# Optimization experiments

Measured on AMD Instinct MI355X. Metric: run time of the kernel, lower is better.

## Reference

```python
import jax, jax.numpy as jnp
import numpy as np


def _sdpa(q, k, v):
    # scaled dot-product attention, no dropout (eval mode)
    d = q.shape[-1]
    s = jnp.einsum('bhqd,bhkd->bhqk', q, k) / jnp.sqrt(jnp.asarray(d, q.dtype))
    a = jax.nn.softmax(s, axis=-1)
    return jnp.einsum('bhqk,bhkd->bhqd', a, v)


def setup_inputs() -> dict:
    key = jax.random.key(0)
    ks = jax.random.split(key, 9)
    BC, H, N, d = 128, 4, 1024, 64
    B, C = 4, 32
    C_ch, l, r, TC = 32, 16, 8, 144
    half_dim = H * d  # 256
    q_t = jax.random.normal(ks[0], (BC, H, N, d), jnp.float32)
    k_t = jax.random.normal(ks[1], (BC, H, N, d), jnp.float32)
    v_t = jax.random.normal(ks[2], (BC, H, N, d), jnp.float32)
    L_n = jax.random.normal(ks[3], (B * N, C_ch, C_ch), jnp.float32)
    slots = jax.random.normal(ks[4], (1, l, half_dim), jnp.float32) * 0.02
    pack_q_w = jax.random.normal(ks[5], (half_dim, half_dim), jnp.float32) * 0.02
    mu_proto_factors = jax.random.normal(ks[6], (l, TC, r), jnp.float32) * 0.02
    spd_beta = jnp.array([0.5], jnp.float32)
    channel_idx = jax.random.randint(ks[7], (C_ch,), 0, TC)
    return dict(q_t=q_t, k_t=k_t, v_t=v_t, L_n=L_n, slots=slots,
                pack_q_w=pack_q_w, mu_proto_factors=mu_proto_factors,
                spd_beta=spd_beta, channel_idx=channel_idx, C=C)


def _spd_distances(L_per_sample, mu_proto_factors, channel_idx):
    # L_per_sample: (B, N, C_ch, C_ch) -> distances (B, l, N)
    B, N, C_ch, _ = L_per_sample.shape
    l = mu_proto_factors.shape[0]
    U_sub = mu_proto_factors[:, channel_idx]            # (l, C_ch, r)
    L_flat = L_per_sample.reshape(B, N, C_ch * C_ch)    # (B, N, C_ch^2)
    L_sqnorm = jnp.sum(L_flat * L_flat, axis=-1)        # (B, N)
    UtU = jnp.einsum('lcr,lcs->lrs', U_sub, U_sub)      # (l, r, r)
    mu_sqnorm = jnp.sum(UtU * UtU, axis=(-2, -1))       # (l,)
    mu_sub = jnp.einsum('lcr,ldr->lcd', U_sub, U_sub)   # (l, C_ch, C_ch)
    mu_flat = mu_sub.reshape(l, C_ch * C_ch)
    cross = jnp.einsum('bni,li->bnl', L_flat, mu_flat)  # (B, N, l)
    dist_sq = L_sqnorm[..., None] + mu_sqnorm[None, None, :] - 2.0 * cross
    dist_sq = jnp.clip(dist_sq, 0.0, None)
    return jnp.sqrt(dist_sq).transpose(0, 2, 1)         # (B, l, N)


def reference(q_t, k_t, v_t, L_n, slots, pack_q_w, mu_proto_factors,
              spd_beta, channel_idx, C):
    BC, H, N, d = q_t.shape
    l = slots.shape[1]
    scale = d ** (-0.5)
    # pack queries: Linear(bias=False) then split heads; slots are shared across batch
    pq = slots[0] @ pack_q_w.T                          # (l, H*d)
    pq = pq.reshape(l, H, d).transpose(1, 0, 2)         # (H, l, d)
    pack_score = jnp.einsum('hld,bhnd->bhln', pq, k_t) * scale  # (BC, H, l, N)
    # SPD geometric bias (L_n is detached in the original)
    B = BC // C
    C_ch = L_n.shape[1]
    L_per_sample = jax.lax.stop_gradient(L_n).reshape(B, N, C_ch, C_ch)
    spd_dist_b = _spd_distances(L_per_sample, mu_proto_factors, channel_idx)  # (B, l, N)
    spd_dist = jnp.repeat(spd_dist_b, C, axis=0)        # (BC, l, N)
    pack_score = pack_score - spd_beta[0] * spd_dist[:, None, :, :]
    pack_attn = jax.nn.softmax(pack_score, axis=-1)
    packed = jnp.einsum('bhln,bhnd->bhld', pack_attn, v_t)  # (BC, H, l, d)
    processed = _sdpa(packed, packed, packed)               # (BC, H, l, d)
    out = _sdpa(q_t, processed, processed)                  # (BC, H, N, d)
    return out
```

## Files before the change

### kernel.cpp

```cpp
#include <hip/hip_runtime.h>
#include <hip/hip_bf16.h>

typedef unsigned short ushort_t;

__device__ __forceinline__ float bf2f(ushort_t u) {
    return __uint_as_float(((unsigned int)u) << 16);
}
__device__ __forceinline__ ushort_t f2bf(float f) {
    __hip_bfloat16 h = __float2bfloat16(f);
    return *reinterpret_cast<ushort_t*>(&h);
}

__global__ __launch_bounds__(256) void k_pq(const float* __restrict__ slots,
                                            const float* __restrict__ W,
                                            float* __restrict__ pq) {
    int l = blockIdx.x, j = threadIdx.x;
    __shared__ float SL[256];
    SL[j] = slots[l * 256 + j];
    __syncthreads();
    const float4* wr = (const float4*)(W + j * 256);
    float acc = 0.f;
#pragma unroll 8
    for (int g = 0; g < 64; ++g) {
        float4 wv = wr[g];
        const float* sl = &SL[g * 4];
        acc += wv.x * sl[0] + wv.y * sl[1] + wv.z * sl[2] + wv.w * sl[3];
    }
    int h = j >> 6, d = j & 63;
    pq[(h * 16 + l) * 64 + d] = acc;
}

__global__ void k_mu(const float* __restrict__ mu,
                     const int* __restrict__ cidx,
                     float* __restrict__ mu_flat,
                     float* __restrict__ mu_sq) {
    int l = blockIdx.x;
    __shared__ float U[256];
    __shared__ float utu[64];
    int t = threadIdx.x;
    {
        int c = t >> 3, r = t & 7;
        U[t] = mu[(l * 144 + cidx[c]) * 8 + r];
    }
    __syncthreads();
#pragma unroll
    for (int i = 0; i < 4; ++i) {
        int e = t + i * 256;
        int c = e >> 5, dd = e & 31;
        float acc = 0.f;
#pragma unroll
        for (int r = 0; r < 8; ++r) acc += U[c * 8 + r] * U[dd * 8 + r];
        mu_flat[l * 1024 + e] = acc;
    }
    if (t < 64) {
        int r = t >> 3, s = t & 7;
        float acc = 0.f;
        for (int c = 0; c < 32; ++c) acc += U[c * 8 + r] * U[c * 8 + s];
        utu[t] = acc;
    }
    __syncthreads();
    if (t == 0) {
        float acc = 0.f;
        for (int i = 0; i < 64; ++i) acc += utu[i] * utu[i];
        mu_sq[l] = acc;
    }
}

__global__ __launch_bounds__(256) void k_dist(const float* __restrict__ Ln,
                                              const float* __restrict__ mu_flat,
                                              const float* __restrict__ mu_sq,
                                              float* __restrict__ dist) {
    int blk = blockIdx.x;
    int nchunk = blk & 63, bs = blk >> 6;
    int t = threadIdx.x;
    int ln = t & 15, rid = t >> 4;
    int n = nchunk * 16 + rid;
    const float4* lr = (const float4*)(Ln + ((size_t)(bs * 1024 + n)) * 1024);
    const float4* mf = (const float4*)mu_flat;
    float lsq = 0.f;
    float cr[16];
#pragma unroll
    for (int l = 0; l < 16; ++l) cr[l] = 0.f;
#pragma unroll 2
    for (int g = 0; g < 16; ++g) {
        float4 lv = lr[g * 16 + ln];
        lsq += lv.x * lv.x + lv.y * lv.y + lv.z * lv.z + lv.w * lv.w;
#pragma unroll
        for (int l = 0; l < 16; ++l) {
            float4 mv = mf[l * 256 + g * 16 + ln];
            cr[l] += lv.x * mv.x + lv.y * mv.y + lv.z * mv.z + lv.w * mv.w;
        }
    }
#pragma unroll
    for (int off = 8; off >= 1; off >>= 1) {
        lsq += __shfl_xor(lsq, off);
#pragma unroll
        for (int l = 0; l < 16; ++l) cr[l] += __shfl_xor(cr[l], off);
    }
    float mycr = cr[0];
#pragma unroll
    for (int l = 1; l < 16; ++l) if (ln == l) mycr = cr[l];
    float d2 = lsq + mu_sq[ln] - 2.f * mycr;
    dist[((size_t)(bs * 16 + ln)) * 1024 + n] = sqrtf(fmaxf(d2, 0.f));
}

__global__ __launch_bounds__(1024) void k_pack2(const float* __restrict__ kt,
                                                const float* __restrict__ vt,
                                                const float* __restrict__ pq,
                                                const float* __restrict__ dist,
                                                const float* __restrict__ beta_p,
                                                float* __restrict__ packed) {
    int bc = blockIdx.x >> 2, h = blockIdx.x & 3;
    int bs = bc >> 5;
    __shared__ __align__(16) float PQ[1024];
    __shared__ __align__(16) ushort_t PB[16 * 1032];
    __shared__ __align__(16) float VST[4096];
    __shared__ float wred[16 * 16];
    __shared__ float gred[16];
    int t = threadIdx.x;
    int lane = t & 63, w = t >> 6;
    PQ[t] = pq[h * 1024 + t];
    float beta = beta_p[0];
    __syncthreads();

    const size_t base = ((size_t)blockIdx.x) * 65536;
    const float4* kr = (const float4*)(kt + base + (size_t)t * 64);
    float sc[16];
#pragma unroll
    for (int l = 0; l < 16; ++l) sc[l] = 0.f;
    for (int g = 0; g < 16; ++g) {
        float4 kv = kr[g];
#pragma unroll
        for (int l = 0; l < 16; ++l) {
            const float* pql = &PQ[l * 64 + g * 4];
            sc[l] += kv.x * pql[0] + kv.y * pql[1] + kv.z * pql[2] + kv.w * pql[3];
        }
    }
#pragma unroll
    for (int l = 0; l < 16; ++l)
        sc[l] = 0.125f * sc[l] - beta * dist[((size_t)(bs * 16 + l)) * 1024 + t];

#pragma unroll
    for (int l = 0; l < 16; ++l) {
        float m = sc[l];
#pragma unroll
        for (int off = 32; off >= 1; off >>= 1) m = fmaxf(m, __shfl_xor(m, off));
        if (lane == 0) wred[l * 16 + w] = m;
    }
    __syncthreads();
    if (t < 16) {
        float m = -1e30f;
#pragma unroll
        for (int w2 = 0; w2 < 16; ++w2) m = fmaxf(m, wred[t * 16 + w2]);
        gred[t] = m;
    }
    __syncthreads();

    float ex[16];
#pragma unroll
    for (int l = 0; l < 16; ++l) {
        ex[l] = __expf(sc[l] - gred[l]);
        float s = ex[l];
#pragma unroll
        for (int off = 32; off >= 1; off >>= 1) s += __shfl_xor(s, off);
        if (lane == 0) wred[l * 16 + w] = s;
    }
    __syncthreads();
    if (t < 16) {
        float s = 0.f;
#pragma unroll
        for (int w2 = 0; w2 < 16; ++w2) s += wred[t * 16 + w2];
        gred[t] = 1.f / s;
    }
    __syncthreads();
#pragma unroll
    for (int l = 0; l < 16; ++l) PB[l * 1032 + t] = f2bf(ex[l] * gred[l]);

    const float4* vr = (const float4*)(vt + base);
    int jg = w >> 2;
    int sl = (w & 3) * 4 + (lane >> 4);
    int dg = lane & 15;
    float4 acc; acc.x = acc.y = acc.z = acc.w = 0.f;
    float4* VST4 = (float4*)VST;
    float4 pre = vr[t];
    for (int ch = 0; ch < 16; ++ch) {
        __syncthreads();
        VST4[t] = pre;
        __syncthreads();
        if (ch < 15) pre = vr[(ch + 1) * 1024 + t];
        const ushort_t* pbp = &PB[sl * 1032 + ch * 64 + jg * 16];
        uint4 pw0 = *(const uint4*)(pbp);
        uint4 pw1 = *(const uint4*)(pbp + 8);
        const float4* vb = VST4 + jg * 256 + dg;
        unsigned wbuf[8] = {pw0.x, pw0.y, pw0.z, pw0.w, pw1.x, pw1.y, pw1.z, pw1.w};
#pragma unroll
        for (int pr = 0; pr < 8; ++pr) {
            float p0 = __uint_as_float(wbuf[pr] << 16);
            float p1 = __uint_as_float(wbuf[pr] & 0xffff0000u);
            float4 v0 = vb[(2 * pr) * 16];
            float4 v1 = vb[(2 * pr + 1) * 16];
            acc.x += p0 * v0.x + p1 * v1.x;
            acc.y += p0 * v0.y + p1 * v1.y;
            acc.z += p0 * v0.z + p1 * v1.z;
            acc.w += p0 * v0.w + p1 * v1.w;
        }
    }
    __syncthreads();
    VST4[jg * 256 + sl * 16 + dg] = acc;
    __syncthreads();
    int l = t >> 6, d = t & 63;
    float sum = VST[l * 64 + d] + VST[1024 + l * 64 + d]
              + VST[2048 + l * 64 + d] + VST[3072 + l * 64 + d];
    packed[((size_t)blockIdx.x) * 1024 + t] = sum;
}

__global__ void k_proc(const float* __restrict__ packed, float* __restrict__ proc) {
    int bh = blockIdx.x;
    __shared__ float P[1024];
    __shared__ float A[256];
    int t = threadIdx.x;
#pragma unroll
    for (int i = 0; i < 4; ++i) P[t + i * 256] = packed[(size_t)bh * 1024 + t + i * 256];
    __syncthreads();
    {
        int i = t >> 4, j = t & 15;
        float acc = 0.f;
#pragma unroll
        for (int dd = 0; dd < 64; ++dd) acc += P[i * 64 + dd] * P[j * 64 + dd];
        A[t] = acc * 0.125f;
    }
    __syncthreads();
    if (t < 16) {
        float m = -1e30f;
#pragma unroll
        for (int j = 0; j < 16; ++j) m = fmaxf(m, A[t * 16 + j]);
        float s = 0.f;
#pragma unroll
        for (int j = 0; j < 16; ++j) { float e = __expf(A[t * 16 + j] - m); A[t * 16 + j] = e; s += e; }
        float inv = 1.f / s;
#pragma unroll
        for (int j = 0; j < 16; ++j) A[t * 16 + j] *= inv;
    }
    __syncthreads();
#pragma unroll
    for (int i = 0; i < 4; ++i) {
        int e = t + i * 256;
        int r = e >> 6, d = e & 63;
        float acc = 0.f;
#pragma unroll
        for (int j = 0; j < 16; ++j) acc += A[r * 16 + j] * P[j * 64 + d];
        proc[(size_t)bh * 1024 + e] = acc;
    }
}

__global__ __launch_bounds__(256) void k_final(const float* __restrict__ qt,
                                               const float* __restrict__ proc,
                                               float* __restrict__ out) {
    int bh = blockIdx.x >> 3, chunk = blockIdx.x & 7;
    __shared__ __align__(16) float P[1024];
    int t = threadIdx.x;
    ((float4*)P)[t] = ((const float4*)(proc + (size_t)bh * 1024))[t];
    __syncthreads();
    int q = t & 3, rid = t >> 2;
    int n0 = chunk * 128 + rid, n1 = n0 + 64;
    const float4* q0 = (const float4*)(qt + ((size_t)bh * 1024 + n0) * 64) + q * 4;
    const float4* q1 = (const float4*)(qt + ((size_t)bh * 1024 + n1) * 64) + q * 4;
    float4 qa0 = q0[0], qa1 = q0[1], qa2 = q0[2], qa3 = q0[3];
    float4 qb0 = q1[0], qb1 = q1[1], qb2 = q1[2], qb3 = q1[3];
    const float4* P4 = (const float4*)P + q * 4;

    float s0[16], s1[16];
#pragma unroll
    for (int j = 0; j < 16; ++j) {
        float4 p0 = P4[j * 16 + 0], p1 = P4[j * 16 + 1];
        float4 p2 = P4[j * 16 + 2], p3 = P4[j * 16 + 3];
        float a = qa0.x * p0.x + qa0.y * p0.y + qa0.z * p0.z + qa0.w * p0.w
                + qa1.x * p1.x + qa1.y * p1.y + qa1.z * p1.z + qa1.w * p1.w
                + qa2.x * p2.x + qa2.y * p2.y + qa2.z * p2.z + qa2.w * p2.w
                + qa3.x * p3.x + qa3.y * p3.y + qa3.z * p3.z + qa3.w * p3.w;
        float b = qb0.x * p0.x + qb0.y * p0.y + qb0.z * p0.z + qb0.w * p0.w
                + qb1.x * p1.x + qb1.y * p1.y + qb1.z * p1.z + qb1.w * p1.w
                + qb2.x * p2.x + qb2.y * p2.y + qb2.z * p2.z + qb2.w * p2.w
                + qb3.x * p3.x + qb3.y * p3.y + qb3.z * p3.z + qb3.w * p3.w;
        a += __shfl_xor(a, 1); a += __shfl_xor(a, 2);
        b += __shfl_xor(b, 1); b += __shfl_xor(b, 2);
        s0[j] = a * 0.125f; s1[j] = b * 0.125f;
    }
    float m0 = s0[0], m1 = s1[0];
#pragma unroll
    for (int j = 1; j < 16; ++j) { m0 = fmaxf(m0, s0[j]); m1 = fmaxf(m1, s1[j]); }
    float t0 = 0.f, t1 = 0.f;
#pragma unroll
    for (int j = 0; j < 16; ++j) {
        s0[j] = __expf(s0[j] - m0); t0 += s0[j];
        s1[j] = __expf(s1[j] - m1); t1 += s1[j];
    }
    float i0 = 1.f / t0, i1 = 1.f / t1;
#pragma unroll
    for (int j = 0; j < 16; ++j) { s0[j] *= i0; s1[j] *= i1; }

    float4 o00, o01, o02, o03, o10, o11, o12, o13;
    o00.x=o00.y=o00.z=o00.w=0.f; o01=o00; o02=o00; o03=o00;
    o10=o00; o11=o00; o12=o00; o13=o00;
#pragma unroll
    for (int j = 0; j < 16; ++j) {
        float4 p0 = P4[j * 16 + 0], p1 = P4[j * 16 + 1];
        float4 p2 = P4[j * 16 + 2], p3 = P4[j * 16 + 3];
        float a = s0[j], b = s1[j];
        o00.x += a * p0.x; o00.y += a * p0.y; o00.z += a * p0.z; o00.w += a * p0.w;
        o01.x += a * p1.x; o01.y += a * p1.y; o01.z += a * p1.z; o01.w += a * p1.w;
        o02.x += a * p2.x; o02.y += a * p2.y; o02.z += a * p2.z; o02.w += a * p2.w;
        o03.x += a * p3.x; o03.y += a * p3.y; o03.z += a * p3.z; o03.w += a * p3.w;
        o10.x += b * p0.x; o10.y += b * p0.y; o10.z += b * p0.z; o10.w += b * p0.w;
        o11.x += b * p1.x; o11.y += b * p1.y; o11.z += b * p1.z; o11.w += b * p1.w;
        o12.x += b * p2.x; o12.y += b * p2.y; o12.z += b * p2.z; o12.w += b * p2.w;
        o13.x += b * p3.x; o13.y += b * p3.y; o13.z += b * p3.z; o13.w += b * p3.w;
    }
    float4* w0 = (float4*)(out + ((size_t)bh * 1024 + n0) * 64) + q * 4;
    float4* w1 = (float4*)(out + ((size_t)bh * 1024 + n1) * 64) + q * 4;
    w0[0] = o00; w0[1] = o01; w0[2] = o02; w0[3] = o03;
    w1[0] = o10; w1[1] = o11; w1[2] = o12; w1[3] = o13;
}

extern "C" void kernel_launch(void* const* d_in, const int* in_sizes, int n_in,
                              void* d_out, int out_size, void* d_ws, size_t ws_size,
                              hipStream_t stream) {
    const float* q     = (const float*)d_in[0];
    const float* k     = (const float*)d_in[1];
    const float* v     = (const float*)d_in[2];
    const float* Ln    = (const float*)d_in[3];
    const float* slots = (const float*)d_in[4];
    const float* W     = (const float*)d_in[5];
    const float* mu    = (const float*)d_in[6];
    const float* beta  = (const float*)d_in[7];
    const int* cidx    = (const int*)d_in[8];

    float* ws     = (float*)d_ws;
    float* pq     = ws;
    float* muf    = ws + 4096;
    float* musq   = ws + 20480;
    float* dist   = ws + 20496;
    float* packed = ws + 86032;
    float* proc   = ws + 610320;

    k_pq   <<<16,   256, 0, stream>>>(slots, W, pq);
    k_mu   <<<16,   256, 0, stream>>>(mu, cidx, muf, musq);
    k_dist <<<256,  256, 0, stream>>>(Ln, muf, musq, dist);
    k_pack2<<<512, 1024, 0, stream>>>(k, v, pq, dist, beta, packed);
    k_proc <<<512,  256, 0, stream>>>(packed, proc);
    k_final<<<4096, 256, 0, stream>>>(q, proc, (float*)d_out);
}
```

Measured before the change: 600.3 us.

## Split pack attention into score and PV kernels, drop max-subtraction softmax

The fused pack kernel is split in two. One kernel computes pack scores over 256-token chunks (2048 blocks), writes the unnormalized exponentials to a global buffer and records partial sums. A second kernel does the P·V product straight from global memory and divides by the summed partials. The k_dist kernel is also re-parallelized with one wavefront per row and lanes split over prototypes. This is meant to raise parallelism and remove the block-wide max/sum reductions and LDS staging, at the cost of an extra global round trip of the probabilities. Skipping the max subtraction risks overflow for large scores, and the probability buffer may fall back to aliasing the output buffer when workspace is small.

```diff
diff --git a/kernel.cpp b/kernel.cpp
--- a/kernel.cpp
+++ b/kernel.cpp
@@ -2,14 +2,6 @@
 #include <hip/hip_bf16.h>
 
 typedef unsigned short ushort_t;
-
-__device__ __forceinline__ float bf2f(ushort_t u) {
-    return __uint_as_float(((unsigned int)u) << 16);
-}
-__device__ __forceinline__ ushort_t f2bf(float f) {
-    __hip_bfloat16 h = __float2bfloat16(f);
-    return *reinterpret_cast<ushort_t*>(&h);
-}
 
 __global__ __launch_bounds__(256) void k_pq(const float* __restrict__ slots,
                                             const float* __restrict__ W,
@@ -71,147 +63,128 @@
                                               const float* __restrict__ mu_sq,
                                               float* __restrict__ dist) {
     int blk = blockIdx.x;
-    int nchunk = blk & 63, bs = blk >> 6;
-    int t = threadIdx.x;
-    int ln = t & 15, rid = t >> 4;
-    int n = nchunk * 16 + rid;
-    const float4* lr = (const float4*)(Ln + ((size_t)(bs * 1024 + n)) * 1024);
-    const float4* mf = (const float4*)mu_flat;
-    float lsq = 0.f;
-    float cr[16];
-#pragma unroll
-    for (int l = 0; l < 16; ++l) cr[l] = 0.f;
-#pragma unroll 2
-    for (int g = 0; g < 16; ++g) {
-        float4 lv = lr[g * 16 + ln];
+    int chunk = blk & 255, bs = blk >> 8;
+    int t = threadIdx.x;
+    int rid = t >> 6, lane = t & 63;
+    int l = lane >> 2, cs = lane & 3;
+    int n = chunk * 4 + rid;
+    const float4* L4 = (const float4*)(Ln + ((size_t)(bs * 1024 + n)) * 1024) + cs * 64;
+    const float4* M4 = (const float4*)mu_flat + l * 256 + cs * 64;
+    float cr = 0.f, lsq = 0.f;
+#pragma unroll 8
+    for (int i = 0; i < 64; ++i) {
+        float4 lv = L4[i];
+        float4 mv = M4[i];
+        cr  += lv.x * mv.x + lv.y * mv.y + lv.z * mv.z + lv.w * mv.w;
         lsq += lv.x * lv.x + lv.y * lv.y + lv.z * lv.z + lv.w * lv.w;
+    }
+    cr  += __shfl_xor(cr, 1);  cr  += __shfl_xor(cr, 2);
+    lsq += __shfl_xor(lsq, 1); lsq += __shfl_xor(lsq, 2);
+    if (cs == 0) {
+        float d2 = lsq + mu_sq[l] - 2.f * cr;
+        dist[((size_t)(bs * 16 + l)) * 1024 + n] = sqrtf(fmaxf(d2, 0.f));
+    }
+}
+
+__global__ __launch_bounds__(256) void k_score(const float* __restrict__ kt,
+                                               const float* __restrict__ pq,
+                                               const float* __restrict__ dist,
+                                               const float* __restrict__ beta_p,
+                                               float* __restrict__ pbuf,
+                                               float* __restrict__ psum) {
+    int bx = blockIdx.x;
+    int nq = bx & 3, bh = bx >> 2;
+    int h = bh & 3;
+    int bs = bh >> 7;
+    __shared__ __align__(16) float PQ[1024];
+    __shared__ float wsum[64];
+    int t = threadIdx.x;
+    int lane = t & 63, w = t >> 6;
+    ((float4*)PQ)[t] = ((const float4*)(pq + h * 1024))[t & 255];
+    float beta = beta_p[0];
+    __syncthreads();
+
+    int n = nq * 256 + t;
+    const float4* kr = (const float4*)(kt + ((size_t)bh) * 65536 + (size_t)n * 64);
+    float sc[16];
+#pragma unroll
+    for (int l = 0; l < 16; ++l) sc[l] = 0.f;
+#pragma unroll
+    for (int gb = 0; gb < 4; ++gb) {
+        float4 kv0 = kr[gb * 4 + 0];
+        float4 kv1 = kr[gb * 4 + 1];
+        float4 kv2 = kr[gb * 4 + 2];
+        float4 kv3 = kr[gb * 4 + 3];
 #pragma unroll
         for (int l = 0; l < 16; ++l) {
-            float4 mv = mf[l * 256 + g * 16 + ln];
-            cr[l] += lv.x * mv.x + lv.y * mv.y + lv.z * mv.z + lv.w * mv.w;
+            const float* p = &PQ[l * 64 + gb * 16];
+            sc[l] += kv0.x * p[0]  + kv0.y * p[1]  + kv0.z * p[2]  + kv0.w * p[3]
+                   + kv1.x * p[4]  + kv1.y * p[5]  + kv1.z * p[6]  + kv1.w * p[7]
+                   + kv2.x * p[8]  + kv2.y * p[9]  + kv2.z * p[10] + kv2.w * p[11]
+                   + kv3.x * p[12] + kv3.y * p[13] + kv3.z * p[14] + kv3.w * p[15];
         }
     }
 #pragma unroll
-    for (int off = 8; off >= 1; off >>= 1) {
-        lsq += __shfl_xor(lsq, off);
-#pragma unroll
-        for (int l = 0; l < 16; ++l) cr[l] += __shfl_xor(cr[l], off);
-    }
-    float mycr = cr[0];
-#pragma unroll
-    for (int l = 1; l < 16; ++l) if (ln == l) mycr = cr[l];
-    float d2 = lsq + mu_sq[ln] - 2.f * mycr;
-    dist[((size_t)(bs * 16 + ln)) * 1024 + n] = sqrtf(fmaxf(d2, 0.f));
-}
-
-__global__ __launch_bounds__(1024) void k_pack2(const float* __restrict__ kt,
-                                                const float* __restrict__ vt,
-                                                const float* __restrict__ pq,
-                                                const float* __restrict__ dist,
-                                                const float* __restrict__ beta_p,
-                                                float* __restrict__ packed) {
-    int bc = blockIdx.x >> 2, h = blockIdx.x & 3;
-    int bs = bc >> 5;
-    __shared__ __align__(16) float PQ[1024];
-    __shared__ __align__(16) ushort_t PB[16 * 1032];
-    __shared__ __align__(16) float VST[4096];
-    __shared__ float wred[16 * 16];
-    __shared__ float gred[16];
+    for (int l = 0; l < 16; ++l) {
+        float e = __expf(0.125f * sc[l] - beta * dist[((size_t)(bs * 16 + l)) * 1024 + n]);
+        sc[l] = e;
+        pbuf[((size_t)(bh * 16 + l)) * 1024 + n] = e;
+    }
+#pragma unroll
+    for (int l = 0; l < 16; ++l) {
+        float s = sc[l];
+#pragma unroll
+        for (int off = 32; off >= 1; off >>= 1) s += __shfl_xor(s, off);
+        if (lane == 0) wsum[l * 4 + w] = s;
+    }
+    __syncthreads();
+    if (t < 16)
+        psum[((size_t)(bh * 16 + t)) * 4 + nq] =
+            wsum[t * 4 + 0] + wsum[t * 4 + 1] + wsum[t * 4 + 2] + wsum[t * 4 + 3];
+}
+
+__global__ __launch_bounds__(1024) void k_pv(const float* __restrict__ vt,
+                                             const float* __restrict__ pbuf,
+                                             const float* __restrict__ psum,
+                                             float* __restrict__ packed) {
+    int bh = blockIdx.x;
+    __shared__ __align__(16) float RED[4096];
     int t = threadIdx.x;
     int lane = t & 63, w = t >> 6;
-    PQ[t] = pq[h * 1024 + t];
-    float beta = beta_p[0];
-    __syncthreads();
-
-    const size_t base = ((size_t)blockIdx.x) * 65536;
-    const float4* kr = (const float4*)(kt + base + (size_t)t * 64);
-    float sc[16];
-#pragma unroll
-    for (int l = 0; l < 16; ++l) sc[l] = 0.f;
-    for (int g = 0; g < 16; ++g) {
-        float4 kv = kr[g];
-#pragma unroll
-        for (int l = 0; l < 16; ++l) {
-            const float* pql = &PQ[l * 64 + g * 4];
-            sc[l] += kv.x * pql[0] + kv.y * pql[1] + kv.z * pql[2] + kv.w * pql[3];
-        }
-    }
-#pragma unroll
-    for (int l = 0; l < 16; ++l)
-        sc[l] = 0.125f * sc[l] - beta * dist[((size_t)(bs * 16 + l)) * 1024 + t];
-
-#pragma unroll
-    for (int l = 0; l < 16; ++l) {
-        float m = sc[l];
-#pragma unroll
-        for (int off = 32; off >= 1; off >>= 1) m = fmaxf(m, __shfl_xor(m, off));
-        if (lane == 0) wred[l * 16 + w] = m;
-    }
-    __syncthreads();
-    if (t < 16) {
-        float m = -1e30f;
-#pragma unroll
-        for (int w2 = 0; w2 < 16; ++w2) m = fmaxf(m, wred[t * 16 + w2]);
-        gred[t] = m;
-    }
-    __syncthreads();
-
-    float ex[16];
-#pragma unroll
-    for (int l = 0; l < 16; ++l) {
-        ex[l] = __expf(sc[l] - gred[l]);
-        float s = ex[l];
-#pragma unroll
-        for (int off = 32; off >= 1; off >>= 1) s += __shfl_xor(s, off);
-        if (lane == 0) wred[l * 16 + w] = s;
-    }
-    __syncthreads();
-    if (t < 16) {
-        float s = 0.f;
-#pragma unroll
-        for (int w2 = 0; w2 < 16; ++w2) s += wred[t * 16 + w2];
-        gred[t] = 1.f / s;
-    }
-    __syncthreads();
-#pragma unroll
-    for (int l = 0; l < 16; ++l) PB[l * 1032 + t] = f2bf(ex[l] * gred[l]);
-
-    const float4* vr = (const float4*)(vt + base);
     int jg = w >> 2;
     int sl = (w & 3) * 4 + (lane >> 4);
     int dg = lane & 15;
+    const float4* pb4 = (const float4*)(pbuf + ((size_t)(bh * 16 + sl)) * 1024 + jg * 256);
+    const float4* v4  = (const float4*)(vt + ((size_t)bh) * 65536) + (size_t)(jg * 256) * 16 + dg;
     float4 acc; acc.x = acc.y = acc.z = acc.w = 0.f;
-    float4* VST4 = (float4*)VST;
-    float4 pre = vr[t];
-    for (int ch = 0; ch < 16; ++ch) {
-        __syncthreads();
-        VST4[t] = pre;
-        __syncthreads();
-        if (ch < 15) pre = vr[(ch + 1) * 1024 + t];
-        const ushort_t* pbp = &PB[sl * 1032 + ch * 64 + jg * 16];
-        uint4 pw0 = *(const uint4*)(pbp);
-        uint4 pw1 = *(const uint4*)(pbp + 8);
-        const float4* vb = VST4 + jg * 256 + dg;
-        unsigned wbuf[8] = {pw0.x, pw0.y, pw0.z, pw0.w, pw1.x, pw1.y, pw1.z, pw1.w};
-#pragma unroll
-        for (int pr = 0; pr < 8; ++pr) {
-            float p0 = __uint_as_float(wbuf[pr] << 16);
-            float p1 = __uint_as_float(wbuf[pr] & 0xffff0000u);
-            float4 v0 = vb[(2 * pr) * 16];
-            float4 v1 = vb[(2 * pr + 1) * 16];
-            acc.x += p0 * v0.x + p1 * v1.x;
-            acc.y += p0 * v0.y + p1 * v1.y;
-            acc.z += p0 * v0.z + p1 * v1.z;
-            acc.w += p0 * v0.w + p1 * v1.w;
-        }
-    }
-    __syncthreads();
-    VST4[jg * 256 + sl * 16 + dg] = acc;
+    for (int rb = 0; rb < 32; ++rb) {
+        float4 pA = pb4[rb * 2 + 0];
+        float4 pB = pb4[rb * 2 + 1];
+        float4 v0 = v4[(rb * 8 + 0) * 16];
+        float4 v1 = v4[(rb * 8 + 1) * 16];
+        float4 v2 = v4[(rb * 8 + 2) * 16];
+        float4 v3 = v4[(rb * 8 + 3) * 16];
+        float4 v5 = v4[(rb * 8 + 4) * 16];
+        float4 v6 = v4[(rb * 8 + 5) * 16];
+        float4 v7 = v4[(rb * 8 + 6) * 16];
+        float4 v8 = v4[(rb * 8 + 7) * 16];
+        acc.x += pA.x * v0.x + pA.y * v1.x + pA.z * v2.x + pA.w * v3.x
+               + pB.x * v5.x + pB.y * v6.x + pB.z * v7.x + pB.w * v8.x;
+        acc.y += pA.x * v0.y + pA.y * v1.y + pA.z * v2.y + pA.w * v3.y
+               + pB.x * v5.y + pB.y * v6.y + pB.z * v7.y + pB.w * v8.y;
+        acc.z += pA.x * v0.z + pA.y * v1.z + pA.z * v2.z + pA.w * v3.z
+               + pB.x * v5.z + pB.y * v6.z + pB.z * v7.z + pB.w * v8.z;
+        acc.w += pA.x * v0.w + pA.y * v1.w + pA.z * v2.w + pA.w * v3.w
+               + pB.x * v5.w + pB.y * v6.w + pB.z * v7.w + pB.w * v8.w;
+    }
+    ((float4*)RED)[jg * 256 + sl * 16 + dg] = acc;
     __syncthreads();
     int l = t >> 6, d = t & 63;
-    float sum = VST[l * 64 + d] + VST[1024 + l * 64 + d]
-              + VST[2048 + l * 64 + d] + VST[3072 + l * 64 + d];
-    packed[((size_t)blockIdx.x) * 1024 + t] = sum;
+    float S = psum[((size_t)(bh * 16 + l)) * 4 + 0] + psum[((size_t)(bh * 16 + l)) * 4 + 1]
+            + psum[((size_t)(bh * 16 + l)) * 4 + 2] + psum[((size_t)(bh * 16 + l)) * 4 + 3];
+    float sum = RED[l * 64 + d] + RED[1024 + l * 64 + d]
+              + RED[2048 + l * 64 + d] + RED[3072 + l * 64 + d];
+    packed[((size_t)bh) * 1024 + t] = sum / S;
 }
 
 __global__ void k_proc(const float* __restrict__ packed, float* __restrict__ proc) {
@@ -342,11 +315,15 @@
     float* dist   = ws + 20496;
     float* packed = ws + 86032;
     float* proc   = ws + 610320;
+    float* psum   = ws + 1134608;
+    const size_t WS_NEEDED = (size_t)(1167376 + 8388608) * sizeof(float);
+    float* pbuf   = (ws_size >= WS_NEEDED) ? (ws + 1167376) : (float*)d_out;
 
     k_pq   <<<16,   256, 0, stream>>>(slots, W, pq);
     k_mu   <<<16,   256, 0, stream>>>(mu, cidx, muf, musq);
-    k_dist <<<256,  256, 0, stream>>>(Ln, muf, musq, dist);
-    k_pack2<<<512, 1024, 0, stream>>>(k, v, pq, dist, beta, packed);
+    k_dist <<<1024, 256, 0, stream>>>(Ln, muf, musq, dist);
+    k_score<<<2048, 256, 0, stream>>>(k, pq, dist, beta, pbuf, psum);
+    k_pv   <<<512, 1024, 0, stream>>>(v, pbuf, psum, packed);
     k_proc <<<512,  256, 0, stream>>>(packed, proc);
     k_final<<<4096, 256, 0, stream>>>(q, proc, (float*)d_out);
 }
```

After: 640.0 us. 6.6% more time.
